# Optimization experiments

Hardware: AMD Instinct MI355X
Metric: run time of the kernel (lower is better)

The kernel has to match this reference:

```python
import jax, jax.numpy as jnp
import numpy as np

OUT, IN, RANK = 4096, 4096, 256
SUBVEC = 8
N_SUBVECS = OUT * RANK // SUBVEC  # 131072 (same for Vh since IN == OUT here)
NNZ = 262144


def setup_inputs() -> dict:
    key = jax.random.key(0)
    ks = jax.random.split(key, 8)
    x = jax.random.normal(ks[0], (4, 128, IN), dtype=jnp.float32)
    U_indices = jax.random.randint(ks[1], (N_SUBVECS,), 0, 256, dtype=jnp.int32)
    U_codebook = jax.random.normal(ks[2], (256, SUBVEC), dtype=jnp.float32)
    S = jax.random.uniform(ks[3], (RANK,), dtype=jnp.float32)
    Vh_indices = jax.random.randint(ks[4], (N_SUBVECS,), 0, 256, dtype=jnp.int32)
    Vh_codebook = jax.random.normal(ks[5], (256, SUBVEC), dtype=jnp.float32)
    residual_indices = jax.random.randint(ks[6], (NNZ,), 0, OUT * IN, dtype=jnp.int32)
    residual_values = jax.random.normal(ks[7], (NNZ,), dtype=jnp.float32)
    return {
        "x": x,
        "U_indices": U_indices,
        "U_codebook": U_codebook,
        "S": S,
        "Vh_indices": Vh_indices,
        "Vh_codebook": Vh_codebook,
        "residual_indices": residual_indices,
        "residual_values": residual_values,
    }


def reference(x, U_indices, U_codebook, S, Vh_indices, Vh_codebook,
              residual_indices, residual_values):
    # Codebook gather -> flatten -> reshape to factor shape (dims divide evenly,
    # so torch's flat[:n] truncation is a no-op here).
    U = U_codebook[U_indices].reshape(OUT, RANK)      # [out, rank]
    Vh = Vh_codebook[Vh_indices].reshape(RANK, IN)    # [rank, in]
    # U @ diag(S) @ Vh, fused as column-scale of U
    weight = (U * S[None, :]) @ Vh                    # [out, in]
    # sparse residual scatter-add into the flat weight
    weight = weight.reshape(-1).at[residual_indices].add(residual_values)
    weight = weight.reshape(OUT, IN)
    # F.linear(x, weight) == x @ weight.T (bias is None)
    return jnp.einsum("bsi,oi->bso", x, weight)
```

## Files before the change

### kernel.cpp

```cpp
#include <hip/hip_runtime.h>
#include <hip/hip_bf16.h>
#include <stdint.h>

#define IN_DIM   4096
#define OUT_DIM  4096
#define RANK     256
#define MROWS    512
#define NNZ_CNT  262144
#define BCAP     128
#define CSTRIDE  16

typedef __attribute__((ext_vector_type(8))) short bf16x8;
typedef __attribute__((ext_vector_type(4))) float f32x4;

#define WS_VHB  ((size_t)0)
#define WS_USB  (WS_VHB + (size_t)RANK * IN_DIM * 2)
#define WS_XT   (WS_USB + (size_t)OUT_DIM * RANK * 2)
#define WS_T    (WS_XT  + (size_t)IN_DIM * MROWS * 2)
#define WS_CUR  (WS_T   + (size_t)MROWS * RANK * 4)
#define WS_KVB  (WS_CUR + (size_t)OUT_DIM * CSTRIDE * 4)

__device__ inline uint4 pack8(float4 a, float4 b) {
    union { __hip_bfloat16 h[8]; uint4 u; } w;
    w.h[0] = __float2bfloat16(a.x); w.h[1] = __float2bfloat16(a.y);
    w.h[2] = __float2bfloat16(a.z); w.h[3] = __float2bfloat16(a.w);
    w.h[4] = __float2bfloat16(b.x); w.h[5] = __float2bfloat16(b.y);
    w.h[6] = __float2bfloat16(b.z); w.h[7] = __float2bfloat16(b.w);
    return w.u;
}

__device__ inline float bfbits(uint32_t lo16) {
    union { uint32_t u; float f; } w; w.u = lo16 << 16; return w.f;
}

__device__ inline void fma8(float* acc, uint4 u, float v) {
    acc[0] += v * bfbits(u.x & 0xffffu);
    acc[1] += v * bfbits(u.x >> 16);
    acc[2] += v * bfbits(u.y & 0xffffu);
    acc[3] += v * bfbits(u.y >> 16);
    acc[4] += v * bfbits(u.z & 0xffffu);
    acc[5] += v * bfbits(u.z >> 16);
    acc[6] += v * bfbits(u.w & 0xffffu);
    acc[7] += v * bfbits(u.w >> 16);
}

__global__ __launch_bounds__(256) void prep_kernel(
    const int*   __restrict__ uidx, const float* __restrict__ ucode,
    const float* __restrict__ S,
    const int*   __restrict__ vidx, const float* __restrict__ vcode,
    __hip_bfloat16* __restrict__ Vhb, __hip_bfloat16* __restrict__ Usb,
    int* __restrict__ cursor, float* __restrict__ tbuf)
{
    const int bid = blockIdx.x;
    const int t   = threadIdx.x;

    if (bid < 256) {
        int base = bid * 512;
        #pragma unroll
        for (int q = 0; q < 2; q++) {
            int sv = base + q * 256 + t;
            int cb = vidx[sv];
            const float4* vc = (const float4*)(vcode + (size_t)cb * 8);
            *(uint4*)(Vhb + (size_t)sv * 8) = pack8(vc[0], vc[1]);
        }
    } else {
        int base = (bid - 256) * 512;
        #pragma unroll
        for (int q = 0; q < 2; q++) {
            int sv = base + q * 256 + t;
            int cb = uidx[sv];
            int r0 = (sv & 31) * 8;
            const float4* uc = (const float4*)(ucode + (size_t)cb * 8);
            const float4* sp = (const float4*)(S + r0);
            float4 a = uc[0], b = uc[1], sa = sp[0], sb = sp[1];
            a.x *= sa.x; a.y *= sa.y; a.z *= sa.z; a.w *= sa.w;
            b.x *= sb.x; b.y *= sb.y; b.z *= sb.z; b.w *= sb.w;
            *(uint4*)(Usb + (size_t)sv * 8) = pack8(a, b);
        }
        cursor[(bid - 256) * 256 + t] = 0;
    }
    tbuf[bid * 256 + t] = 0.f;
}

__global__ __launch_bounds__(256) void mid_kernel(
    const int* __restrict__ ridx, const float* __restrict__ rval,
    int* __restrict__ cursor, int2* __restrict__ kvb,
    const float* __restrict__ x,
    const __hip_bfloat16* __restrict__ Vhb,
    float* __restrict__ tbuf,
    __hip_bfloat16* __restrict__ xT)
{
    __shared__ __align__(16) char smem[18432];
    const int t = threadIdx.x;

    if (blockIdx.x < 256) {
        typedef __hip_bfloat16 bfrow[72];
        bfrow* As = (bfrow*)smem;
        bfrow* Bs = (bfrow*)(smem + 9216);

        const int bid = blockIdx.x;
        const int ks = bid & 7, nb = (bid >> 3) & 3, mb = bid >> 5;
        const int m0 = mb * 64, n0 = nb * 64, kbase = ks * 512;
        const int lane = t & 63, wave = t >> 6;
        const int wm = wave >> 1, wn = wave & 1;
        const int l15 = lane & 15, l4 = lane >> 4;
        const int srow = t >> 2, sg = t & 3;

        f32x4 acc[2][2];
        #pragma unroll
        for (int i = 0; i < 2; i++)
            #pragma unroll
            for (int j = 0; j < 2; j++) acc[i][j] = (f32x4){0.f, 0.f, 0.f, 0.f};

        for (int s = 0; s < 8; s++) {
            int k0 = kbase + s * 64;
            const float* xp = x + (size_t)(m0 + srow) * IN_DIM + k0 + sg * 16;
            *(uint4*)&As[srow][sg * 16] =
                pack8(*(const float4*)xp, *(const float4*)(xp + 4));
            *(uint4*)&As[srow][sg * 16 + 8] =
                pack8(*(const float4*)(xp + 8), *(const float4*)(xp + 12));
            const __hip_bfloat16* bp =
                Vhb + (size_t)(n0 + srow) * IN_DIM + k0 + sg * 16;
            *(uint4*)&Bs[srow][sg * 16]     = *(const uint4*)bp;
            *(uint4*)&Bs[srow][sg * 16 + 8] = *(const uint4*)(bp + 8);
            __syncthreads();
            #pragma unroll
            for (int kk = 0; kk < 2; kk++) {
                bf16x8 a[2], b[2];
                #pragma unroll
                for (int i = 0; i < 2; i++)
                    a[i] = *(const bf16x8*)&As[wm * 32 + i * 16 + l15][kk * 32 + l4 * 8];
                #pragma unroll
                for (int j = 0; j < 2; j++)
                    b[j] = *(const bf16x8*)&Bs[wn * 32 + j * 16 + l15][kk * 32 + l4 * 8];
                #pragma unroll
                for (int i = 0; i < 2; i++)
                    #pragma unroll
                    for (int j = 0; j < 2; j++)
                        acc[i][j] = __builtin_amdgcn_mfma_f32_16x16x32_bf16(
                            a[i], b[j], acc[i][j], 0, 0, 0);
            }
            __syncthreads();
        }

        #pragma unroll
        for (int i = 0; i < 2; i++)
            #pragma unroll
            for (int j = 0; j < 2; j++)
                #pragma unroll
                for (int q = 0; q < 4; q++) {
                    int row = m0 + wm * 32 + i * 16 + l4 * 4 + q;
                    int col = n0 + wn * 32 + j * 16 + l15;
                    atomicAdd(&tbuf[row * RANK + col], acc[i][j][q]);
                }
    } else if (blockIdx.x < 1280) {
        int k = (blockIdx.x - 256) * 256 + t;
        int idx = ridx[k];
        int o = idx >> 12, i = idx & 4095;
        int pos = atomicAdd(&cursor[o * CSTRIDE], 1);
        if (pos < BCAP)
            kvb[(size_t)o * BCAP + pos] = make_int2(i, __float_as_int(rval[k]));
    } else {
        float (*tile)[65] = (float(*)[65])smem;
        const int tb = blockIdx.x - 1280;
        const int i0 = (tb >> 3) * 64;
        const int m0 = (tb & 7) * 64;
        const int rr = t >> 4, c4 = t & 15;
        #pragma unroll
        for (int p = 0; p < 4; p++) {
            int r = p * 16 + rr;
            float4 v = *(const float4*)(x + (size_t)(m0 + r) * IN_DIM + i0 + c4 * 4);
            tile[r][c4 * 4 + 0] = v.x;
            tile[r][c4 * 4 + 1] = v.y;
            tile[r][c4 * 4 + 2] = v.z;
            tile[r][c4 * 4 + 3] = v.w;
        }
        __syncthreads();
        #pragma unroll
        for (int p = 0; p < 4; p++) {
            int i = p * 16 + rr;
            union { __hip_bfloat16 h[4]; uint2 u; } w;
            w.h[0] = __float2bfloat16(tile[c4 * 4 + 0][i]);
            w.h[1] = __float2bfloat16(tile[c4 * 4 + 1][i]);
            w.h[2] = __float2bfloat16(tile[c4 * 4 + 2][i]);
            w.h[3] = __float2bfloat16(tile[c4 * 4 + 3][i]);
            *(uint2*)(xT + (size_t)(i0 + i) * MROWS + m0 + c4 * 4) = w.u;
        }
    }
}

__global__ __launch_bounds__(512) void gemm2_sparse_kernel(
    const float* __restrict__ tbuf,
    const __hip_bfloat16* __restrict__ Usb,
    const int* __restrict__ cursor,
    const int2* __restrict__ kvb,
    const __hip_bfloat16* __restrict__ xT,
    float* __restrict__ out)
{
    __shared__ __align__(16) char smem[18432];
    typedef __hip_bfloat16 bfrow[72];
    bfrow* As = (bfrow*)smem;
    bfrow* Bs = (bfrow*)(smem + 9216);
    float (*sacc)[65] = (float(*)[65])smem;

    const int bid = blockIdx.x;
    const int mb = bid & 7, nb = bid >> 3;
    const int m0 = mb * 64, n0 = nb * 64;
    const int t = threadIdx.x;
    const int lane = t & 63, wave = t >> 6;
    const int wm = wave >> 2, wn = wave & 3;
    const int l15 = lane & 15, l4 = lane >> 4;

    f32x4 acc[2];
    acc[0] = (f32x4){0.f, 0.f, 0.f, 0.f};
    acc[1] = (f32x4){0.f, 0.f, 0.f, 0.f};

    {
        const int srow = t >> 3, sg = t & 7;
        for (int s = 0; s < 4; s++) {
            int k0 = s * 64;
            const float* tp = tbuf + (size_t)(m0 + srow) * RANK + k0 + sg * 8;
            *(uint4*)&As[srow][sg * 8] =
                pack8(*(const float4*)tp, *(const float4*)(tp + 4));
            const __hip_bfloat16* bp =
                Usb + (size_t)(n0 + srow) * RANK + k0 + sg * 8;
            *(uint4*)&Bs[srow][sg * 8] = *(const uint4*)bp;
            __syncthreads();
            #pragma unroll
            for (int kk = 0; kk < 2; kk++) {
                bf16x8 a[2], b;
                #pragma unroll
                for (int i = 0; i < 2; i++)
                    a[i] = *(const bf16x8*)&As[wm * 32 + i * 16 + l15][kk * 32 + l4 * 8];
                b = *(const bf16x8*)&Bs[wn * 16 + l15][kk * 32 + l4 * 8];
                #pragma unroll
                for (int i = 0; i < 2; i++)
                    acc[i] = __builtin_amdgcn_mfma_f32_16x16x32_bf16(
                        a[i], b, acc[i], 0, 0, 0);
            }
            __syncthreads();
        }
    }

    {
        const int orel = t >> 3;
        const int ms   = t & 7;
        const int o    = n0 + orel;
        int cnt = cursor[o * CSTRIDE]; cnt = cnt < BCAP ? cnt : BCAP;
        const int2* kp  = kvb + (size_t)o * BCAP;
        const int4* kp4 = (const int4*)kp;
        const __hip_bfloat16* xm = xT + m0 + ms * 8;

        float r[8];
        #pragma unroll
        for (int j = 0; j < 8; j++) r[j] = 0.f;

        int k = 0;
        for (; k + 8 <= cnt; k += 8) {
            int4 e0 = kp4[(k >> 1) + 0], e1 = kp4[(k >> 1) + 1];
            int4 e2 = kp4[(k >> 1) + 2], e3 = kp4[(k >> 1) + 3];
            uint4 u0 = *(const uint4*)(xm + (size_t)e0.x * MROWS);
            uint4 u1 = *(const uint4*)(xm + (size_t)e0.z * MROWS);
            uint4 u2 = *(const uint4*)(xm + (size_t)e1.x * MROWS);
            uint4 u3 = *(const uint4*)(xm + (size_t)e1.z * MROWS);
            uint4 u4 = *(const uint4*)(xm + (size_t)e2.x * MROWS);
            uint4 u5 = *(const uint4*)(xm + (size_t)e2.z * MROWS);
            uint4 u6 = *(const uint4*)(xm + (size_t)e3.x * MROWS);
            uint4 u7 = *(const uint4*)(xm + (size_t)e3.z * MROWS);
            fma8(r, u0, __int_as_float(e0.y));
            fma8(r, u1, __int_as_float(e0.w));
            fma8(r, u2, __int_as_float(e1.y));
            fma8(r, u3, __int_as_float(e1.w));
            fma8(r, u4, __int_as_float(e2.y));
            fma8(r, u5, __int_as_float(e2.w));
            fma8(r, u6, __int_as_float(e3.y));
            fma8(r, u7, __int_as_float(e3.w));
        }
        if (k + 4 <= cnt) {
            int4 e0 = kp4[(k >> 1) + 0], e1 = kp4[(k >> 1) + 1];
            uint4 u0 = *(const uint4*)(xm + (size_t)e0.x * MROWS);
            uint4 u1 = *(const uint4*)(xm + (size_t)e0.z * MROWS);
            uint4 u2 = *(const uint4*)(xm + (size_t)e1.x * MROWS);
            uint4 u3 = *(const uint4*)(xm + (size_t)e1.z * MROWS);
            fma8(r, u0, __int_as_float(e0.y));
            fma8(r, u1, __int_as_float(e0.w));
            fma8(r, u2, __int_as_float(e1.y));
            fma8(r, u3, __int_as_float(e1.w));
            k += 4;
        }
        for (; k < cnt; k++) {
            int2 e = kp[k];
            uint4 u = *(const uint4*)(xm + (size_t)e.x * MROWS);
            fma8(r, u, __int_as_float(e.y));
        }

        __syncthreads();
        *(float4*)&sacc[orel][ms * 8]     = make_float4(r[0], r[1], r[2], r[3]);
        *(float4*)&sacc[orel][ms * 8 + 4] = make_float4(r[4], r[5], r[6], r[7]);
    }
    __syncthreads();

    #pragma unroll
    for (int i = 0; i < 2; i++)
        #pragma unroll
        for (int q = 0; q < 4; q++) {
            int rrel = wm * 32 + i * 16 + l4 * 4 + q;
            int crel = wn * 16 + l15;
            out[(size_t)(m0 + rrel) * OUT_DIM + n0 + crel] =
                acc[i][q] + sacc[crel][rrel];
        }
}

extern "C" void kernel_launch(void* const* d_in, const int* in_sizes, int n_in,
                              void* d_out, int out_size, void* d_ws, size_t ws_size,
                              hipStream_t stream)
{
    const float* x    = (const float*)d_in[0];
    const int*   uidx = (const int*)  d_in[1];
    const float* ucb  = (const float*)d_in[2];
    const float* S    = (const float*)d_in[3];
    const int*   vidx = (const int*)  d_in[4];
    const float* vcb  = (const float*)d_in[5];
    const int*   ridx = (const int*)  d_in[6];
    const float* rval = (const float*)d_in[7];
    float* out = (float*)d_out;

    char* ws = (char*)d_ws;
    __hip_bfloat16* Vhb  = (__hip_bfloat16*)(ws + WS_VHB);
    __hip_bfloat16* Usb  = (__hip_bfloat16*)(ws + WS_USB);
    __hip_bfloat16* xT   = (__hip_bfloat16*)(ws + WS_XT);
    float*          tbuf = (float*)(ws + WS_T);
    int*            cur  = (int*)(ws + WS_CUR);
    int2*           kvb  = (int2*)(ws + WS_KVB);

    prep_kernel<<<dim3(512), dim3(256), 0, stream>>>(
        uidx, ucb, S, vidx, vcb, Vhb, Usb, cur, tbuf);

    mid_kernel<<<dim3(1792), dim3(256), 0, stream>>>(
        ridx, rval, cur, kvb, x, Vhb, tbuf, xT);

    gemm2_sparse_kernel<<<dim3(512), dim3(512), 0, stream>>>(
        tbuf, Usb, cur, kvb, xT, out);
}
```

Before: 58.29 us.

## Split gemm2 block into MFMA waves and sparse-gather waves running concurrently

Within the second GEMM kernel, the first four waves now do the low-rank MFMA product, reading operands directly from global memory into registers instead of staging them in LDS. The other four waves run the sparse residual gather at the same time, each thread handling 16 rows instead of 8. The two groups meet at one barrier through a shared accumulator tile, and the MFMA waves write the final output. This is meant to overlap the compute-bound and latency-bound phases and to drop the LDS staging barriers. In exchange, half the threads take part in each phase, global loads in the MFMA path are uncoalesced, and each MFMA wave does more work.

```diff
diff --git a/kernel.cpp b/kernel.cpp
--- a/kernel.cpp
+++ b/kernel.cpp
@@ -197,118 +197,119 @@
     const __hip_bfloat16* __restrict__ xT,
     float* __restrict__ out)
 {
-    __shared__ __align__(16) char smem[18432];
-    typedef __hip_bfloat16 bfrow[72];
-    bfrow* As = (bfrow*)smem;
-    bfrow* Bs = (bfrow*)(smem + 9216);
-    float (*sacc)[65] = (float(*)[65])smem;
+    __shared__ __align__(16) float sacc[64][65];
 
     const int bid = blockIdx.x;
     const int mb = bid & 7, nb = bid >> 3;
     const int m0 = mb * 64, n0 = nb * 64;
     const int t = threadIdx.x;
     const int lane = t & 63, wave = t >> 6;
-    const int wm = wave >> 2, wn = wave & 3;
     const int l15 = lane & 15, l4 = lane >> 4;
 
-    f32x4 acc[2];
-    acc[0] = (f32x4){0.f, 0.f, 0.f, 0.f};
-    acc[1] = (f32x4){0.f, 0.f, 0.f, 0.f};
-
-    {
-        const int srow = t >> 3, sg = t & 7;
-        for (int s = 0; s < 4; s++) {
-            int k0 = s * 64;
-            const float* tp = tbuf + (size_t)(m0 + srow) * RANK + k0 + sg * 8;
-            *(uint4*)&As[srow][sg * 8] =
-                pack8(*(const float4*)tp, *(const float4*)(tp + 4));
-            const __hip_bfloat16* bp =
-                Usb + (size_t)(n0 + srow) * RANK + k0 + sg * 8;
-            *(uint4*)&Bs[srow][sg * 8] = *(const uint4*)bp;
-            __syncthreads();
-            #pragma unroll
-            for (int kk = 0; kk < 2; kk++) {
-                bf16x8 a[2], b;
-                #pragma unroll
-                for (int i = 0; i < 2; i++)
-                    a[i] = *(const bf16x8*)&As[wm * 32 + i * 16 + l15][kk * 32 + l4 * 8];
-                b = *(const bf16x8*)&Bs[wn * 16 + l15][kk * 32 + l4 * 8];
-                #pragma unroll
-                for (int i = 0; i < 2; i++)
-                    acc[i] = __builtin_amdgcn_mfma_f32_16x16x32_bf16(
-                        a[i], b, acc[i], 0, 0, 0);
+    if (wave < 4) {
+        const int wm = wave >> 1, wn = wave & 1;
+        f32x4 acc[2][2];
+        #pragma unroll
+        for (int i = 0; i < 2; i++)
+            #pragma unroll
+            for (int j = 0; j < 2; j++) acc[i][j] = (f32x4){0.f, 0.f, 0.f, 0.f};
+
+        for (int s = 0; s < 8; s++) {
+            int k0 = s * 32 + l4 * 8;
+            bf16x8 a[2], b[2];
+            #pragma unroll
+            for (int i = 0; i < 2; i++) {
+                const float* tp =
+                    tbuf + (size_t)(m0 + wm * 32 + i * 16 + l15) * RANK + k0;
+                uint4 p = pack8(*(const float4*)tp, *(const float4*)(tp + 4));
+                a[i] = *(bf16x8*)&p;
             }
-            __syncthreads();
-        }
-    }
-
-    {
-        const int orel = t >> 3;
-        const int ms   = t & 7;
+            #pragma unroll
+            for (int j = 0; j < 2; j++) {
+                const __hip_bfloat16* bp =
+                    Usb + (size_t)(n0 + wn * 32 + j * 16 + l15) * RANK + k0;
+                uint4 p = *(const uint4*)bp;
+                b[j] = *(bf16x8*)&p;
+            }
+            #pragma unroll
+            for (int i = 0; i < 2; i++)
+                #pragma unroll
+                for (int j = 0; j < 2; j++)
+                    acc[i][j] = __builtin_amdgcn_mfma_f32_16x16x32_bf16(
+                        a[i], b[j], acc[i][j], 0, 0, 0);
+        }
+
+        __syncthreads();
+
+        #pragma unroll
+        for (int i = 0; i < 2; i++)
+            #pragma unroll
+            for (int j = 0; j < 2; j++)
+                #pragma unroll
+                for (int q = 0; q < 4; q++) {
+                    int rrel = wm * 32 + i * 16 + l4 * 4 + q;
+                    int crel = wn * 32 + j * 16 + l15;
+                    out[(size_t)(m0 + rrel) * OUT_DIM + n0 + crel] =
+                        acc[i][j][q] + sacc[crel][rrel];
+                }
+    } else {
+        const int ts   = t - 256;
+        const int orel = ts >> 2;
+        const int ms   = ts & 3;
         const int o    = n0 + orel;
         int cnt = cursor[o * CSTRIDE]; cnt = cnt < BCAP ? cnt : BCAP;
         const int2* kp  = kvb + (size_t)o * BCAP;
         const int4* kp4 = (const int4*)kp;
-        const __hip_bfloat16* xm = xT + m0 + ms * 8;
-
-        float r[8];
-        #pragma unroll
-        for (int j = 0; j < 8; j++) r[j] = 0.f;
+        const __hip_bfloat16* xm = xT + m0 + ms * 16;
+
+        float r[16];
+        #pragma unroll
+        for (int j = 0; j < 16; j++) r[j] = 0.f;
 
         int k = 0;
-        for (; k + 8 <= cnt; k += 8) {
+        for (; k + 4 <= cnt; k += 4) {
             int4 e0 = kp4[(k >> 1) + 0], e1 = kp4[(k >> 1) + 1];
-            int4 e2 = kp4[(k >> 1) + 2], e3 = kp4[(k >> 1) + 3];
-            uint4 u0 = *(const uint4*)(xm + (size_t)e0.x * MROWS);
-            uint4 u1 = *(const uint4*)(xm + (size_t)e0.z * MROWS);
-            uint4 u2 = *(const uint4*)(xm + (size_t)e1.x * MROWS);
-            uint4 u3 = *(const uint4*)(xm + (size_t)e1.z * MROWS);
-            uint4 u4 = *(const uint4*)(xm + (size_t)e2.x * MROWS);
-            uint4 u5 = *(const uint4*)(xm + (size_t)e2.z * MROWS);
-            uint4 u6 = *(const uint4*)(xm + (size_t)e3.x * MROWS);
-            uint4 u7 = *(const uint4*)(xm + (size_t)e3.z * MROWS);
-            fma8(r, u0, __int_as_float(e0.y));
-            fma8(r, u1, __int_as_float(e0.w));
-            fma8(r, u2, __int_as_float(e1.y));
-            fma8(r, u3, __int_as_float(e1.w));
-            fma8(r, u4, __int_as_float(e2.y));
-            fma8(r, u5, __int_as_float(e2.w));
-            fma8(r, u6, __int_as_float(e3.y));
-            fma8(r, u7, __int_as_float(e3.w));
-        }
-        if (k + 4 <= cnt) {
-            int4 e0 = kp4[(k >> 1) + 0], e1 = kp4[(k >> 1) + 1];
-            uint4 u0 = *(const uint4*)(xm + (size_t)e0.x * MROWS);
-            uint4 u1 = *(const uint4*)(xm + (size_t)e0.z * MROWS);
-            uint4 u2 = *(const uint4*)(xm + (size_t)e1.x * MROWS);
-            uint4 u3 = *(const uint4*)(xm + (size_t)e1.z * MROWS);
-            fma8(r, u0, __int_as_float(e0.y));
-            fma8(r, u1, __int_as_float(e0.w));
-            fma8(r, u2, __int_as_float(e1.y));
-            fma8(r, u3, __int_as_float(e1.w));
-            k += 4;
-        }
-        for (; k < cnt; k++) {
+            const __hip_bfloat16* p0 = xm + (size_t)e0.x * MROWS;
+            const __hip_bfloat16* p1 = xm + (size_t)e0.z * MROWS;
+            const __hip_bfloat16* p2 = xm + (size_t)e1.x * MROWS;
+            const __hip_bfloat16* p3 = xm + (size_t)e1.z * MROWS;
+            uint4 a0 = *(const uint4*)p0, b0 = *(const uint4*)(p0 + 8);
+            uint4 a1 = *(const uint4*)p1, b1 = *(const uint4*)(p1 + 8);
+            uint4 a2 = *(const uint4*)p2, b2 = *(const uint4*)(p2 + 8);
+            uint4 a3 = *(const uint4*)p3, b3 = *(const uint4*)(p3 + 8);
+            float v0 = __int_as_float(e0.y), v1 = __int_as_float(e0.w);
+            float v2 = __int_as_float(e1.y), v3 = __int_as_float(e1.w);
+            fma8(r, a0, v0); fma8(r + 8, b0, v0);
+            fma8(r, a1, v1); fma8(r + 8, b1, v1);
+            fma8(r, a2, v2); fma8(r + 8, b2, v2);
+            fma8(r, a3, v3); fma8(r + 8, b3, v3);
+        }
+        if (k + 2 <= cnt) {
+            int4 e0 = kp4[k >> 1];
+            const __hip_bfloat16* p0 = xm + (size_t)e0.x * MROWS;
+            const __hip_bfloat16* p1 = xm + (size_t)e0.z * MROWS;
+            uint4 a0 = *(const uint4*)p0, b0 = *(const uint4*)(p0 + 8);
+            uint4 a1 = *(const uint4*)p1, b1 = *(const uint4*)(p1 + 8);
+            float v0 = __int_as_float(e0.y), v1 = __int_as_float(e0.w);
+            fma8(r, a0, v0); fma8(r + 8, b0, v0);
+            fma8(r, a1, v1); fma8(r + 8, b1, v1);
+            k += 2;
+        }
+        if (k < cnt) {
             int2 e = kp[k];
-            uint4 u = *(const uint4*)(xm + (size_t)e.x * MROWS);
-            fma8(r, u, __int_as_float(e.y));
-        }
+            const __hip_bfloat16* p0 = xm + (size_t)e.x * MROWS;
+            uint4 a0 = *(const uint4*)p0, b0 = *(const uint4*)(p0 + 8);
+            float v0 = __int_as_float(e.y);
+            fma8(r, a0, v0); fma8(r + 8, b0, v0);
+        }
+
+        #pragma unroll
+        for (int j = 0; j < 4; j++)
+            *(float4*)&sacc[orel][ms * 16 + j * 4] =
+                make_float4(r[j * 4], r[j * 4 + 1], r[j * 4 + 2], r[j * 4 + 3]);
 
         __syncthreads();
-        *(float4*)&sacc[orel][ms * 8]     = make_float4(r[0], r[1], r[2], r[3]);
-        *(float4*)&sacc[orel][ms * 8 + 4] = make_float4(r[4], r[5], r[6], r[7]);
     }
-    __syncthreads();
-
-    #pragma unroll
-    for (int i = 0; i < 2; i++)
-        #pragma unroll
-        for (int q = 0; q < 4; q++) {
-            int rrel = wm * 32 + i * 16 + l4 * 4 + q;
-            int crel = wn * 16 + l15;
-            out[(size_t)(m0 + rrel) * OUT_DIM + n0 + crel] =
-                acc[i][q] + sacc[crel][rrel];
-        }
 }
 
 extern "C" void kernel_launch(void* const* d_in, const int* in_sizes, int n_in,
```

Result: slower. 64.75 us (+11.1%).
